# Kernel tuning notes

Hardware: AMD Instinct MI355X
Metric: run time of the kernel (lower is better)

## Reference

```python
import jax, jax.numpy as jnp
import numpy as np

EPS = 0.07      # sinkhorn temperature
ITERS = 7       # sinkhorn iterations
TINY = 1e-8
NORM_EPS = 1e-12  # F.normalize default clamp


def setup_inputs() -> dict:
    key = jax.random.key(0)
    k1, k2 = jax.random.split(key)
    x = jax.random.normal(k1, (64, 2048, 24, 12), dtype=jnp.float32)
    anchors = jax.random.normal(k2, (2, 2048), dtype=jnp.float32) * 0.02
    return {"x": x, "anchors": anchors}


def reference(x, anchors):
    B, C, H, W = x.shape
    HW = H * W
    # tokens: (B, HW, C)
    X = x.reshape(B, C, HW).transpose(0, 2, 1)
    Xn = X / jnp.maximum(jnp.linalg.norm(X, axis=-1, keepdims=True), NORM_EPS)
    An = anchors / jnp.maximum(jnp.linalg.norm(anchors, axis=-1, keepdims=True), NORM_EPS)
    # cosine cost (B, HW, 2)
    Cmat = 1.0 - jnp.einsum('bhc,kc->bhk', Xn, An)
    Kmat = jnp.exp(-Cmat / max(EPS, TINY)) + TINY
    a = jnp.full((B, HW), 1.0 / HW, dtype=Kmat.dtype)
    b = jnp.full((B, 2), 0.5, dtype=Kmat.dtype)

    def step(carry, _):
        u, v = carry
        Kv = jnp.einsum('bhk,bk->bh', Kmat, v) + TINY
        u = a / Kv
        KTu = jnp.einsum('bhk,bh->bk', Kmat, u) + TINY
        v = b / KTu
        return (u, v), None

    u0 = jnp.ones((B, HW), dtype=Kmat.dtype)
    v0 = jnp.ones((B, 2), dtype=Kmat.dtype)
    (u, v), _ = jax.lax.scan(step, (u0, v0), None, length=ITERS)
    # transport plan and soft masks
    P = Kmat * u[:, :, None] * v[:, None, :]          # (B, HW, 2)
    m = (P * HW).transpose(0, 2, 1).reshape(B, 2, H, W)
    # masked pooling for both prototypes at once
    num = jnp.einsum('bchw,bkhw->bkc', x, m)           # (B, 2, C)
    den = m.sum(axis=(2, 3)) + 1e-6                    # (B, 2)
    c = num / den[:, :, None]
    c0_vec = c[:, 0][:, :, None, None]                 # (B, C, 1, 1)
    c1_vec = c[:, 1][:, :, None, None]
    return (c0_vec, c1_vec, m)
```

## Files before the change

### kernel.cpp

```cpp
#include <hip/hip_runtime.h>

#define B_    64
#define C_    2048
#define HW_   288
#define EPS_  0.07f
#define TINY_ 1e-8f
#define NCH_  64
#define CPC_  (C_ / NCH_)
#define NGRP_ 16

__device__ __forceinline__ float comp(const float4 v, int i) {
  return i == 0 ? v.x : i == 1 ? v.y : i == 2 ? v.z : v.w;
}

__device__ __forceinline__ void acc3(const float4 v, float a0, float a1,
                                     float* ssq, float* sd0, float* sd1) {
  ssq[0] += v.x * v.x; ssq[1] += v.y * v.y; ssq[2] += v.z * v.z; ssq[3] += v.w * v.w;
  sd0[0] += v.x * a0;  sd0[1] += v.y * a0;  sd0[2] += v.z * a0;  sd0[3] += v.w * a0;
  sd1[0] += v.x * a1;  sd1[1] += v.y * a1;  sd1[2] += v.z * a1;  sd1[3] += v.w * a1;
}

__global__ __launch_bounds__(256) void k1_partials(
    const float* __restrict__ x, const float* __restrict__ anchors,
    float* __restrict__ part) {
  __shared__ float4 lds[4][3][72];

  int bi = blockIdx.x;
  int b  = bi >> 4;
  int cg = bi & 15;
  int t = threadIdx.x, lane = t & 63, wid = t >> 6;
  int ch = cg * 4 + wid;
  int c0 = ch * CPC_;
  const float* xb = x + ((size_t)b * C_ + c0) * HW_;
  const float4* a0v = (const float4*)(anchors + c0);
  const float4* a1v = (const float4*)(anchors + C_ + c0);

  float ssq[4] = {0,0,0,0}, sd0[4] = {0,0,0,0}, sd1[4] = {0,0,0,0};

  float4 xbuf[4], abuf0, abuf1;
#pragma unroll
  for (int j = 0; j < 4; ++j)
    xbuf[j] = ((const float4*)(xb + (size_t)j * HW_))[lane];
  abuf0 = a0v[0];
  abuf1 = a1v[0];

#pragma unroll 1
  for (int r = 0; r < CPC_; r += 4) {
    float4 xcur[4], ac0 = abuf0, ac1 = abuf1;
#pragma unroll
    for (int j = 0; j < 4; ++j) xcur[j] = xbuf[j];
    if (r + 4 < CPC_) {
#pragma unroll
      for (int j = 0; j < 4; ++j)
        xbuf[j] = ((const float4*)(xb + (size_t)(r + 4 + j) * HW_))[lane];
      abuf0 = a0v[(r >> 2) + 1];
      abuf1 = a1v[(r >> 2) + 1];
    }
#pragma unroll
    for (int j = 0; j < 4; ++j)
      acc3(xcur[j], comp(ac0, j), comp(ac1, j), ssq, sd0, sd1);
  }

  int rg = lane >> 3, q = lane & 7;
  float4 tv[4];
  float ta0[4], ta1[4];
#pragma unroll
  for (int k = 0; k < CPC_ / 8; ++k) {
    int r = k * 8 + rg;
    tv[k]  = ((const float4*)(xb + (size_t)r * HW_))[64 + q];
    ta0[k] = anchors[c0 + r];
    ta1[k] = anchors[C_ + c0 + r];
  }
  float tsq[4] = {0,0,0,0}, td0[4] = {0,0,0,0}, td1[4] = {0,0,0,0};
#pragma unroll
  for (int k = 0; k < CPC_ / 8; ++k)
    acc3(tv[k], ta0[k], ta1[k], tsq, td0, td1);
#pragma unroll
  for (int off = 8; off < 64; off <<= 1) {
#pragma unroll
    for (int j = 0; j < 4; ++j) {
      tsq[j] += __shfl_xor(tsq[j], off);
      td0[j] += __shfl_xor(td0[j], off);
      td1[j] += __shfl_xor(td1[j], off);
    }
  }

  lds[wid][0][lane] = make_float4(ssq[0], ssq[1], ssq[2], ssq[3]);
  lds[wid][1][lane] = make_float4(sd0[0], sd0[1], sd0[2], sd0[3]);
  lds[wid][2][lane] = make_float4(sd1[0], sd1[1], sd1[2], sd1[3]);
  if (lane < 8) {
    lds[wid][0][64 + lane] = make_float4(tsq[0], tsq[1], tsq[2], tsq[3]);
    lds[wid][1][64 + lane] = make_float4(td0[0], td0[1], td0[2], td0[3]);
    lds[wid][2][64 + lane] = make_float4(td1[0], td1[1], td1[2], td1[3]);
  }
  __syncthreads();

  if (t < 216) {
    int p = t / 72, i = t - p * 72;
    float4 s0 = lds[0][p][i], s1 = lds[1][p][i];
    float4 s2 = lds[2][p][i], s3 = lds[3][p][i];
    float4 s = make_float4(s0.x + s1.x + s2.x + s3.x,
                           s0.y + s1.y + s2.y + s3.y,
                           s0.z + s1.z + s2.z + s3.z,
                           s0.w + s1.w + s2.w + s3.w);
    ((float4*)(part + ((size_t)(b * NGRP_ + cg) * 3 + p) * HW_))[i] = s;
  }
}

__device__ __forceinline__ void block_reduce2(
    float& p0, float& p1, volatile float* red0, volatile float* red1,
    int t, int nw) {
  int lane = t & 63, wid = t >> 6;
#pragma unroll
  for (int off = 32; off >= 1; off >>= 1) {
    p0 += __shfl_down(p0, off);
    p1 += __shfl_down(p1, off);
  }
  __syncthreads();
  if (lane == 0) { red0[wid] = p0; red1[wid] = p1; }
  __syncthreads();
  float s0 = 0.f, s1 = 0.f;
  for (int w = 0; w < nw; ++w) { s0 += red0[w]; s1 += red1[w]; }
  p0 = s0; p1 = s1;
}

__global__ __launch_bounds__(320) void k2_sinkhorn(
    const float* __restrict__ part, const float* __restrict__ anchors,
    float* __restrict__ out_m, float* __restrict__ invden) {
  int b = blockIdx.x, t = threadIdx.x;
  __shared__ float red0[8], red1[8];
  const int nw = 5;

  float a0 = 0.f, a1 = 0.f;
  for (int c = t; c < C_; c += 320) {
    float q0 = anchors[c], q1 = anchors[C_ + c];
    a0 += q0 * q0; a1 += q1 * q1;
  }
  block_reduce2(a0, a1, red0, red1, t, nw);
  float ian0 = 1.0f / fmaxf(sqrtf(a0), 1e-12f);
  float ian1 = 1.0f / fmaxf(sqrtf(a1), 1e-12f);

  float K0 = 0.f, K1 = 0.f;
  if (t < HW_) {
    const float* p = part + (size_t)b * NGRP_ * 3 * HW_ + t;
    float ssq = 0.f, d0 = 0.f, d1 = 0.f;
#pragma unroll
    for (int g = 0; g < NGRP_; ++g) {
      const float* q = p + (size_t)g * 3 * HW_;
      ssq += q[0];
      d0  += q[HW_];
      d1  += q[2 * HW_];
    }
    float ixn = 1.0f / fmaxf(sqrtf(ssq), 1e-12f);
    K0 = expf((d0 * ixn * ian0 - 1.0f) / EPS_) + TINY_;
    K1 = expf((d1 * ixn * ian1 - 1.0f) / EPS_) + TINY_;
  }

  float v0 = 1.f, v1 = 1.f, u = 0.f;
  for (int it = 0; it < 7; ++it) {
    if (t < HW_) u = (1.0f / (float)HW_) / (K0 * v0 + K1 * v1 + TINY_);
    float p0 = K0 * u, p1 = K1 * u;
    block_reduce2(p0, p1, red0, red1, t, nw);
    v0 = 0.5f / (p0 + TINY_);
    v1 = 0.5f / (p1 + TINY_);
  }

  float m0 = 0.f, m1 = 0.f;
  if (t < HW_) {
    m0 = K0 * u * v0 * (float)HW_;
    m1 = K1 * u * v1 * (float)HW_;
  }
  float q0 = m0, q1 = m1;
  block_reduce2(q0, q1, red0, red1, t, nw);
  if (t < HW_) {
    out_m[(b * 2 + 0) * HW_ + t] = m0;
    out_m[(b * 2 + 1) * HW_ + t] = m1;
  }
  if (t == 0) {
    invden[b * 2 + 0] = 1.0f / (q0 + 1e-6f);
    invden[b * 2 + 1] = 1.0f / (q1 + 1e-6f);
  }
}

__global__ __launch_bounds__(256) void k3_pool(
    const float* __restrict__ x, const float* __restrict__ m,
    const float* __restrict__ invden, float* __restrict__ out) {
  int bi = blockIdx.x;
  int b = bi >> 4, seg = bi & 15;
  int t = threadIdx.x, oct = t & 7, rl = t >> 3;

  const float4* m0 = (const float4*)(m + (b * 2 + 0) * HW_);
  const float4* m1 = (const float4*)(m + (b * 2 + 1) * HW_);
  float4 w0[9], w1[9];
#pragma unroll
  for (int j = 0; j < 9; ++j) {
    w0[j] = m0[oct + 8 * j];
    w1[j] = m1[oct + 8 * j];
  }
  float inv0 = invden[2 * b], inv1 = invden[2 * b + 1];

  int cbase = seg * 128;
#pragma unroll 1
  for (int g = 0; g < 4; ++g) {
    int c = cbase + g * 32 + rl;
    const float4* xr = (const float4*)(x + ((size_t)b * C_ + c) * HW_);
    float4 xa[9];
#pragma unroll
    for (int j = 0; j < 9; ++j) xa[j] = xr[oct + 8 * j];
    float a0 = 0.f, a1 = 0.f;
#pragma unroll
    for (int j = 0; j < 9; ++j) {
      a0 += xa[j].x * w0[j].x + xa[j].y * w0[j].y + xa[j].z * w0[j].z + xa[j].w * w0[j].w;
      a1 += xa[j].x * w1[j].x + xa[j].y * w1[j].y + xa[j].z * w1[j].z + xa[j].w * w1[j].w;
    }
#pragma unroll
    for (int off = 4; off >= 1; off >>= 1) {
      a0 += __shfl_xor(a0, off);
      a1 += __shfl_xor(a1, off);
    }
    if (oct == 0) {
      out[(size_t)b * C_ + c] = a0 * inv0;
      out[(size_t)B_ * C_ + (size_t)b * C_ + c] = a1 * inv1;
    }
  }
}

extern "C" void kernel_launch(void* const* d_in, const int* in_sizes, int n_in,
                              void* d_out, int out_size, void* d_ws, size_t ws_size,
                              hipStream_t stream) {
  const float* x       = (const float*)d_in[0];
  const float* anchors = (const float*)d_in[1];
  float* out = (float*)d_out;

  float* invden = (float*)d_ws;
  float* part = invden + 128;

  float* out_m = out + 2 * B_ * C_;

  k1_partials<<<B_ * (NCH_ / 4), 256, 0, stream>>>(x, anchors, part);
  k2_sinkhorn<<<B_, 320, 0, stream>>>(part, anchors, out_m, invden);
  k3_pool<<<B_ * 16, 256, 0, stream>>>(x, out_m, invden, out);
}
```

Before: 245.7 us.

## Fuse Sinkhorn solve into pooling kernel with redundant per-block recomputation

Merges the Sinkhorn kernel into the pooling kernel. Each of the 16 pooling blocks per batch now recomputes the cost matrix and Sinkhorn iterations from the partials and keeps the mask in LDS, which removes one launch and the global round trip for the mask and inverse denominators. In exchange, the Sinkhorn work and the partial reads are duplicated 16 times, and the serial reduction chain now sits in front of the x streaming in every block.

```diff
diff --git a/kernel.cpp b/kernel.cpp
--- a/kernel.cpp
+++ b/kernel.cpp
@@ -108,8 +108,7 @@
 }
 
 __device__ __forceinline__ void block_reduce2(
-    float& p0, float& p1, volatile float* red0, volatile float* red1,
-    int t, int nw) {
+    float& p0, float& p1, volatile float* red0, volatile float* red1, int t) {
   int lane = t & 63, wid = t >> 6;
 #pragma unroll
   for (int off = 32; off >= 1; off >>= 1) {
@@ -119,85 +118,100 @@
   __syncthreads();
   if (lane == 0) { red0[wid] = p0; red1[wid] = p1; }
   __syncthreads();
-  float s0 = 0.f, s1 = 0.f;
-  for (int w = 0; w < nw; ++w) { s0 += red0[w]; s1 += red1[w]; }
-  p0 = s0; p1 = s1;
-}
-
-__global__ __launch_bounds__(320) void k2_sinkhorn(
-    const float* __restrict__ part, const float* __restrict__ anchors,
-    float* __restrict__ out_m, float* __restrict__ invden) {
-  int b = blockIdx.x, t = threadIdx.x;
-  __shared__ float red0[8], red1[8];
-  const int nw = 5;
-
-  float a0 = 0.f, a1 = 0.f;
-  for (int c = t; c < C_; c += 320) {
-    float q0 = anchors[c], q1 = anchors[C_ + c];
-    a0 += q0 * q0; a1 += q1 * q1;
-  }
-  block_reduce2(a0, a1, red0, red1, t, nw);
-  float ian0 = 1.0f / fmaxf(sqrtf(a0), 1e-12f);
-  float ian1 = 1.0f / fmaxf(sqrtf(a1), 1e-12f);
-
-  float K0 = 0.f, K1 = 0.f;
-  if (t < HW_) {
-    const float* p = part + (size_t)b * NGRP_ * 3 * HW_ + t;
-    float ssq = 0.f, d0 = 0.f, d1 = 0.f;
-#pragma unroll
-    for (int g = 0; g < NGRP_; ++g) {
-      const float* q = p + (size_t)g * 3 * HW_;
-      ssq += q[0];
-      d0  += q[HW_];
-      d1  += q[2 * HW_];
-    }
-    float ixn = 1.0f / fmaxf(sqrtf(ssq), 1e-12f);
-    K0 = expf((d0 * ixn * ian0 - 1.0f) / EPS_) + TINY_;
-    K1 = expf((d1 * ixn * ian1 - 1.0f) / EPS_) + TINY_;
-  }
-
-  float v0 = 1.f, v1 = 1.f, u = 0.f;
-  for (int it = 0; it < 7; ++it) {
-    if (t < HW_) u = (1.0f / (float)HW_) / (K0 * v0 + K1 * v1 + TINY_);
-    float p0 = K0 * u, p1 = K1 * u;
-    block_reduce2(p0, p1, red0, red1, t, nw);
-    v0 = 0.5f / (p0 + TINY_);
-    v1 = 0.5f / (p1 + TINY_);
-  }
-
-  float m0 = 0.f, m1 = 0.f;
-  if (t < HW_) {
-    m0 = K0 * u * v0 * (float)HW_;
-    m1 = K1 * u * v1 * (float)HW_;
-  }
-  float q0 = m0, q1 = m1;
-  block_reduce2(q0, q1, red0, red1, t, nw);
-  if (t < HW_) {
-    out_m[(b * 2 + 0) * HW_ + t] = m0;
-    out_m[(b * 2 + 1) * HW_ + t] = m1;
-  }
-  if (t == 0) {
-    invden[b * 2 + 0] = 1.0f / (q0 + 1e-6f);
-    invden[b * 2 + 1] = 1.0f / (q1 + 1e-6f);
-  }
-}
-
-__global__ __launch_bounds__(256) void k3_pool(
-    const float* __restrict__ x, const float* __restrict__ m,
-    const float* __restrict__ invden, float* __restrict__ out) {
+  p0 = red0[0] + red0[1] + red0[2] + red0[3];
+  p1 = red1[0] + red1[1] + red1[2] + red1[3];
+}
+
+__global__ __launch_bounds__(256) void k23_fused(
+    const float* __restrict__ x, const float* __restrict__ part,
+    const float* __restrict__ anchors, float* __restrict__ out,
+    float* __restrict__ out_m) {
   int bi = blockIdx.x;
   int b = bi >> 4, seg = bi & 15;
   int t = threadIdx.x, oct = t & 7, rl = t >> 3;
 
-  const float4* m0 = (const float4*)(m + (b * 2 + 0) * HW_);
-  const float4* m1 = (const float4*)(m + (b * 2 + 1) * HW_);
+  __shared__ float red0[4], red1[4];
+  __shared__ float sm0[HW_], sm1[HW_];
+
+  const float* p = part + (size_t)b * NGRP_ * 3 * HW_;
+  float ssqa = 0.f, d0a = 0.f, d1a = 0.f;
+#pragma unroll
+  for (int g = 0; g < NGRP_; ++g) {
+    const float* q = p + (size_t)g * 3 * HW_ + t;
+    ssqa += q[0];
+    d0a  += q[HW_];
+    d1a  += q[2 * HW_];
+  }
+  float ssqb = 0.f, d0b = 0.f, d1b = 0.f;
+  if (t < 32) {
+#pragma unroll
+    for (int g = 0; g < NGRP_; ++g) {
+      const float* q = p + (size_t)g * 3 * HW_ + 256 + t;
+      ssqb += q[0];
+      d0b  += q[HW_];
+      d1b  += q[2 * HW_];
+    }
+  }
+
+  float a0 = 0.f, a1 = 0.f;
+  for (int c = t; c < C_; c += 256) {
+    float q0 = anchors[c], q1 = anchors[C_ + c];
+    a0 += q0 * q0; a1 += q1 * q1;
+  }
+  block_reduce2(a0, a1, red0, red1, t);
+  float ian0 = 1.0f / fmaxf(sqrtf(a0), 1e-12f);
+  float ian1 = 1.0f / fmaxf(sqrtf(a1), 1e-12f);
+
+  float ixna = 1.0f / fmaxf(sqrtf(ssqa), 1e-12f);
+  float K0a = expf((d0a * ixna * ian0 - 1.0f) / EPS_) + TINY_;
+  float K1a = expf((d1a * ixna * ian1 - 1.0f) / EPS_) + TINY_;
+  float K0b = 0.f, K1b = 0.f;
+  if (t < 32) {
+    float ixnb = 1.0f / fmaxf(sqrtf(ssqb), 1e-12f);
+    K0b = expf((d0b * ixnb * ian0 - 1.0f) / EPS_) + TINY_;
+    K1b = expf((d1b * ixnb * ian1 - 1.0f) / EPS_) + TINY_;
+  }
+
+  float v0 = 1.f, v1 = 1.f, ua = 0.f, ub = 0.f;
+  for (int it = 0; it < 7; ++it) {
+    ua = (1.0f / (float)HW_) / (K0a * v0 + K1a * v1 + TINY_);
+    ub = (t < 32) ? (1.0f / (float)HW_) / (K0b * v0 + K1b * v1 + TINY_) : 0.f;
+    float p0 = K0a * ua + K0b * ub;
+    float p1 = K1a * ua + K1b * ub;
+    block_reduce2(p0, p1, red0, red1, t);
+    v0 = 0.5f / (p0 + TINY_);
+    v1 = 0.5f / (p1 + TINY_);
+  }
+
+  float m0a = K0a * ua * v0 * (float)HW_;
+  float m1a = K1a * ua * v1 * (float)HW_;
+  float m0b = 0.f, m1b = 0.f;
+  sm0[t] = m0a; sm1[t] = m1a;
+  if (t < 32) {
+    m0b = K0b * ub * v0 * (float)HW_;
+    m1b = K1b * ub * v1 * (float)HW_;
+    sm0[256 + t] = m0b; sm1[256 + t] = m1b;
+  }
+  float q0 = m0a + m0b, q1 = m1a + m1b;
+  block_reduce2(q0, q1, red0, red1, t);
+  float inv0 = 1.0f / (q0 + 1e-6f);
+  float inv1 = 1.0f / (q1 + 1e-6f);
+
+  if (seg == 0) {
+    out_m[(b * 2 + 0) * HW_ + t] = m0a;
+    out_m[(b * 2 + 1) * HW_ + t] = m1a;
+    if (t < 32) {
+      out_m[(b * 2 + 0) * HW_ + 256 + t] = m0b;
+      out_m[(b * 2 + 1) * HW_ + 256 + t] = m1b;
+    }
+  }
+
   float4 w0[9], w1[9];
 #pragma unroll
   for (int j = 0; j < 9; ++j) {
-    w0[j] = m0[oct + 8 * j];
-    w1[j] = m1[oct + 8 * j];
-  }
-  float inv0 = invden[2 * b], inv1 = invden[2 * b + 1];
+    w0[j] = ((const float4*)sm0)[oct + 8 * j];
+    w1[j] = ((const float4*)sm1)[oct + 8 * j];
+  }
 
   int cbase = seg * 128;
 #pragma unroll 1
@@ -207,20 +221,20 @@
     float4 xa[9];
 #pragma unroll
     for (int j = 0; j < 9; ++j) xa[j] = xr[oct + 8 * j];
-    float a0 = 0.f, a1 = 0.f;
+    float a0s = 0.f, a1s = 0.f;
 #pragma unroll
     for (int j = 0; j < 9; ++j) {
-      a0 += xa[j].x * w0[j].x + xa[j].y * w0[j].y + xa[j].z * w0[j].z + xa[j].w * w0[j].w;
-      a1 += xa[j].x * w1[j].x + xa[j].y * w1[j].y + xa[j].z * w1[j].z + xa[j].w * w1[j].w;
+      a0s += xa[j].x * w0[j].x + xa[j].y * w0[j].y + xa[j].z * w0[j].z + xa[j].w * w0[j].w;
+      a1s += xa[j].x * w1[j].x + xa[j].y * w1[j].y + xa[j].z * w1[j].z + xa[j].w * w1[j].w;
     }
 #pragma unroll
     for (int off = 4; off >= 1; off >>= 1) {
-      a0 += __shfl_xor(a0, off);
-      a1 += __shfl_xor(a1, off);
+      a0s += __shfl_xor(a0s, off);
+      a1s += __shfl_xor(a1s, off);
     }
     if (oct == 0) {
-      out[(size_t)b * C_ + c] = a0 * inv0;
-      out[(size_t)B_ * C_ + (size_t)b * C_ + c] = a1 * inv1;
+      out[(size_t)b * C_ + c] = a0s * inv0;
+      out[(size_t)B_ * C_ + (size_t)b * C_ + c] = a1s * inv1;
     }
   }
 }
@@ -232,12 +246,10 @@
   const float* anchors = (const float*)d_in[1];
   float* out = (float*)d_out;
 
-  float* invden = (float*)d_ws;
-  float* part = invden + 128;
+  float* part = (float*)d_ws;
 
   float* out_m = out + 2 * B_ * C_;
 
   k1_partials<<<B_ * (NCH_ / 4), 256, 0, stream>>>(x, anchors, part);
-  k2_sinkhorn<<<B_, 320, 0, stream>>>(part, anchors, out_m, invden);
-  k3_pool<<<B_ * 16, 256, 0, stream>>>(x, out_m, invden, out);
-}
+  k23_fused<<<B_ * 16, 256, 0, stream>>>(x, part, anchors, out, out_m);
+}
```

Result: no change. 246.2 us (+0.2%).

## Fuse sinkhorn into partials kernel via last-block atomic counter

Applied to the files above, without the earlier changes.

Removes the separate per-batch sinkhorn kernel. The last of the 16 partial blocks for each batch, detected with an atomic counter and threadfence, runs the sinkhorn iterations in a single wavefront using shuffle reductions only. A tiny init kernel precomputes the anchor norms and zeroes the counters. The trade is one extra small launch plus serialized tail work inside k1, against dropping one kernel launch and the cross-wave LDS syncs.

```diff
diff --git a/kernel.cpp b/kernel.cpp
--- a/kernel.cpp
+++ b/kernel.cpp
@@ -20,9 +20,37 @@
   sd1[0] += v.x * a1;  sd1[1] += v.y * a1;  sd1[2] += v.z * a1;  sd1[3] += v.w * a1;
 }
 
+__global__ __launch_bounds__(256) void k0_init(
+    const float* __restrict__ anchors, unsigned* __restrict__ counters,
+    float* __restrict__ ian) {
+  int t = threadIdx.x, lane = t & 63, wid = t >> 6;
+  __shared__ float red0[4], red1[4];
+  float a0 = 0.f, a1 = 0.f;
+  for (int c = t; c < C_; c += 256) {
+    float q0 = anchors[c], q1 = anchors[C_ + c];
+    a0 += q0 * q0; a1 += q1 * q1;
+  }
+#pragma unroll
+  for (int off = 32; off >= 1; off >>= 1) {
+    a0 += __shfl_down(a0, off);
+    a1 += __shfl_down(a1, off);
+  }
+  if (lane == 0) { red0[wid] = a0; red1[wid] = a1; }
+  __syncthreads();
+  if (t == 0) {
+    float s0 = red0[0] + red0[1] + red0[2] + red0[3];
+    float s1 = red1[0] + red1[1] + red1[2] + red1[3];
+    ian[0] = 1.0f / fmaxf(sqrtf(s0), 1e-12f);
+    ian[1] = 1.0f / fmaxf(sqrtf(s1), 1e-12f);
+  }
+  if (t < B_) counters[t] = 0u;
+}
+
 __global__ __launch_bounds__(256) void k1_partials(
     const float* __restrict__ x, const float* __restrict__ anchors,
-    float* __restrict__ part) {
+    float* __restrict__ part, unsigned* __restrict__ counters,
+    const float* __restrict__ ian, float* __restrict__ out_m,
+    float* __restrict__ invden) {
   __shared__ float4 lds[4][3][72];
 
   int bi = blockIdx.x;
@@ -105,80 +133,77 @@
                            s0.w + s1.w + s2.w + s3.w);
     ((float4*)(part + ((size_t)(b * NGRP_ + cg) * 3 + p) * HW_))[i] = s;
   }
-}
-
-__device__ __forceinline__ void block_reduce2(
-    float& p0, float& p1, volatile float* red0, volatile float* red1,
-    int t, int nw) {
-  int lane = t & 63, wid = t >> 6;
-#pragma unroll
-  for (int off = 32; off >= 1; off >>= 1) {
-    p0 += __shfl_down(p0, off);
-    p1 += __shfl_down(p1, off);
-  }
+
+  __threadfence();
+  __shared__ unsigned sdone;
+  if (t == 0) sdone = atomicAdd(&counters[b], 1u);
   __syncthreads();
-  if (lane == 0) { red0[wid] = p0; red1[wid] = p1; }
-  __syncthreads();
-  float s0 = 0.f, s1 = 0.f;
-  for (int w = 0; w < nw; ++w) { s0 += red0[w]; s1 += red1[w]; }
-  p0 = s0; p1 = s1;
-}
-
-__global__ __launch_bounds__(320) void k2_sinkhorn(
-    const float* __restrict__ part, const float* __restrict__ anchors,
-    float* __restrict__ out_m, float* __restrict__ invden) {
-  int b = blockIdx.x, t = threadIdx.x;
-  __shared__ float red0[8], red1[8];
-  const int nw = 5;
-
-  float a0 = 0.f, a1 = 0.f;
-  for (int c = t; c < C_; c += 320) {
-    float q0 = anchors[c], q1 = anchors[C_ + c];
-    a0 += q0 * q0; a1 += q1 * q1;
-  }
-  block_reduce2(a0, a1, red0, red1, t, nw);
-  float ian0 = 1.0f / fmaxf(sqrtf(a0), 1e-12f);
-  float ian1 = 1.0f / fmaxf(sqrtf(a1), 1e-12f);
-
-  float K0 = 0.f, K1 = 0.f;
-  if (t < HW_) {
-    const float* p = part + (size_t)b * NGRP_ * 3 * HW_ + t;
-    float ssq = 0.f, d0 = 0.f, d1 = 0.f;
-#pragma unroll
-    for (int g = 0; g < NGRP_; ++g) {
-      const float* q = p + (size_t)g * 3 * HW_;
-      ssq += q[0];
-      d0  += q[HW_];
-      d1  += q[2 * HW_];
-    }
-    float ixn = 1.0f / fmaxf(sqrtf(ssq), 1e-12f);
-    K0 = expf((d0 * ixn * ian0 - 1.0f) / EPS_) + TINY_;
-    K1 = expf((d1 * ixn * ian1 - 1.0f) / EPS_) + TINY_;
-  }
-
-  float v0 = 1.f, v1 = 1.f, u = 0.f;
+  if (sdone != NGRP_ - 1) return;
+  if (t >= 64) return;
+  __threadfence();
+
+  const float* p = part + (size_t)b * NGRP_ * 3 * HW_;
+  float ian0 = ian[0], ian1 = ian[1];
+  float K0v[5], K1v[5];
+#pragma unroll
+  for (int j = 0; j < 5; ++j) {
+    int tk = lane + 64 * j;
+    K0v[j] = 0.f; K1v[j] = 0.f;
+    if (tk < HW_) {
+      float ssqs = 0.f, d0s = 0.f, d1s = 0.f;
+#pragma unroll
+      for (int g = 0; g < NGRP_; ++g) {
+        const float* qp = p + (size_t)g * 3 * HW_ + tk;
+        ssqs += qp[0];
+        d0s  += qp[HW_];
+        d1s  += qp[2 * HW_];
+      }
+      float ixn = 1.0f / fmaxf(sqrtf(ssqs), 1e-12f);
+      K0v[j] = expf((d0s * ixn * ian0 - 1.0f) / EPS_) + TINY_;
+      K1v[j] = expf((d1s * ixn * ian1 - 1.0f) / EPS_) + TINY_;
+    }
+  }
+
+  float v0 = 1.f, v1 = 1.f, uv[5];
   for (int it = 0; it < 7; ++it) {
-    if (t < HW_) u = (1.0f / (float)HW_) / (K0 * v0 + K1 * v1 + TINY_);
-    float p0 = K0 * u, p1 = K1 * u;
-    block_reduce2(p0, p1, red0, red1, t, nw);
+    float p0 = 0.f, p1 = 0.f;
+#pragma unroll
+    for (int j = 0; j < 5; ++j) {
+      int tk = lane + 64 * j;
+      uv[j] = (tk < HW_)
+            ? (1.0f / (float)HW_) / (K0v[j] * v0 + K1v[j] * v1 + TINY_) : 0.f;
+      p0 += K0v[j] * uv[j];
+      p1 += K1v[j] * uv[j];
+    }
+#pragma unroll
+    for (int off = 1; off < 64; off <<= 1) {
+      p0 += __shfl_xor(p0, off);
+      p1 += __shfl_xor(p1, off);
+    }
     v0 = 0.5f / (p0 + TINY_);
     v1 = 0.5f / (p1 + TINY_);
   }
 
-  float m0 = 0.f, m1 = 0.f;
-  if (t < HW_) {
-    m0 = K0 * u * v0 * (float)HW_;
-    m1 = K1 * u * v1 * (float)HW_;
-  }
-  float q0 = m0, q1 = m1;
-  block_reduce2(q0, q1, red0, red1, t, nw);
-  if (t < HW_) {
-    out_m[(b * 2 + 0) * HW_ + t] = m0;
-    out_m[(b * 2 + 1) * HW_ + t] = m1;
-  }
-  if (t == 0) {
-    invden[b * 2 + 0] = 1.0f / (q0 + 1e-6f);
-    invden[b * 2 + 1] = 1.0f / (q1 + 1e-6f);
+  float q0 = 0.f, q1 = 0.f;
+#pragma unroll
+  for (int j = 0; j < 5; ++j) {
+    int tk = lane + 64 * j;
+    if (tk < HW_) {
+      float m0 = K0v[j] * uv[j] * v0 * (float)HW_;
+      float m1 = K1v[j] * uv[j] * v1 * (float)HW_;
+      out_m[(b * 2 + 0) * HW_ + tk] = m0;
+      out_m[(b * 2 + 1) * HW_ + tk] = m1;
+      q0 += m0; q1 += m1;
+    }
+  }
+#pragma unroll
+  for (int off = 1; off < 64; off <<= 1) {
+    q0 += __shfl_xor(q0, off);
+    q1 += __shfl_xor(q1, off);
+  }
+  if (lane == 0) {
+    invden[2 * b + 0] = 1.0f / (q0 + 1e-6f);
+    invden[2 * b + 1] = 1.0f / (q1 + 1e-6f);
   }
 }
 
@@ -232,12 +257,15 @@
   const float* anchors = (const float*)d_in[1];
   float* out = (float*)d_out;
 
-  float* invden = (float*)d_ws;
-  float* part = invden + 128;
+  unsigned* counters = (unsigned*)d_ws;
+  float* ian    = (float*)d_ws + 64;
+  float* invden = (float*)d_ws + 72;
+  float* part   = (float*)d_ws + 208;
 
   float* out_m = out + 2 * B_ * C_;
 
-  k1_partials<<<B_ * (NCH_ / 4), 256, 0, stream>>>(x, anchors, part);
-  k2_sinkhorn<<<B_, 320, 0, stream>>>(part, anchors, out_m, invden);
+  k0_init<<<1, 256, 0, stream>>>(anchors, counters, ian);
+  k1_partials<<<B_ * (NCH_ / 4), 256, 0, stream>>>(x, anchors, part, counters,
+                                                   ian, out_m, invden);
   k3_pool<<<B_ * 16, 256, 0, stream>>>(x, out_m, invden, out);
 }
```

After: 437.8 us. 78.2% more time.
